# Kernel tuning notes

Hardware: AMD Instinct MI355X
Metric: run time of the kernel (lower is better)

## Reference

```python
import jax, jax.numpy as jnp
import numpy as np

B, Wd, C, H, F = 48, 88, 256, 32, 1024
NH_SELF, NH_CROSS = 8, 8


def _ln(x, g, b, eps=1e-5):
    mu = x.mean(-1, keepdims=True)
    var = ((x - mu) ** 2).mean(-1, keepdims=True)
    return (x - mu) / jnp.sqrt(var + eps) * g + b


def setup_inputs() -> dict:
    key = jax.random.key(0)
    ks = jax.random.split(key, 16)
    s = 0.02  # weight init scale
    d = {
        'pooled_features': jax.random.normal(ks[0], (B, Wd, C), jnp.float32),
        'features': jax.random.normal(ks[1], (B, C, H, Wd), jnp.float32),
        'self_pe': jax.random.normal(ks[2], (Wd, C), jnp.float32),
        'cross_pe': jax.random.normal(ks[3], (H, C), jnp.float32),
    }
    # LayerNorm params
    for n in ['ln_qs', 'ln_vs', 'ln_qc', 'ln_kv', 'ln_vc', 'ln_ffn']:
        d[n + '_g'] = jnp.ones((C,), jnp.float32)
        d[n + '_b'] = jnp.zeros((C,), jnp.float32)
    # attention projections (stored [in,out]; y = x @ W + b)
    names = ['Wq_s', 'Wk_s', 'Wv_s', 'Wp_s', 'Wq_c', 'Wk_c', 'Wv_c', 'Wp_c']
    for i, n in enumerate(names):
        d[n] = jax.random.normal(ks[4 + i], (C, C), jnp.float32) * s
    for n in ['bq_s', 'bv_s', 'bp_s', 'bq_c', 'bv_c', 'bp_c']:
        d[n] = jnp.zeros((C,), jnp.float32)
    # FFN
    d['W1'] = jax.random.normal(ks[12], (C, F), jnp.float32) * s
    d['b1'] = jnp.zeros((F,), jnp.float32)
    d['W2'] = jax.random.normal(ks[13], (F, C), jnp.float32) * s
    d['b2'] = jnp.zeros((C,), jnp.float32)
    return d


def reference(pooled_features, features, self_pe, cross_pe,
              ln_qs_g, ln_qs_b, ln_vs_g, ln_vs_b,
              ln_qc_g, ln_qc_b, ln_kv_g, ln_kv_b, ln_vc_g, ln_vc_b,
              ln_ffn_g, ln_ffn_b,
              Wq_s, bq_s, Wk_s, Wv_s, bv_s, Wp_s, bp_s,
              Wq_c, bq_c, Wk_c, Wv_c, bv_c, Wp_c, bp_c,
              W1, b1, W2, b2):
    b, w, c = pooled_features.shape
    h = features.shape[2]
    ds = c // NH_SELF
    dc = c // NH_CROSS

    # ---- cross attention first (op_order='cross_first', with_pe=True) ----
    xq = pooled_features                                  # [B,W,C]
    qn = _ln(xq, ln_qc_g, ln_qc_b)
    kv = jnp.transpose(features, (0, 3, 2, 1))            # [B,W,H,C]
    kn = _ln(kv + cross_pe[None, None], ln_kv_g, ln_kv_b)
    vn = _ln(kv, ln_vc_g, ln_vc_b)
    q = (qn @ Wq_c + bq_c).reshape(b, w, NH_CROSS, dc)    # query len 1 per column
    k = (kn @ Wk_c).reshape(b, w, h, NH_CROSS, dc)
    v = (vn @ Wv_c + bv_c).reshape(b, w, h, NH_CROSS, dc)
    attn = jnp.einsum('bwhd,bwkhd->bwhk', q, k) * (dc ** -0.5)
    attn = jax.nn.softmax(attn, axis=-1)
    out = jnp.einsum('bwhk,bwkhd->bwhd', attn, v).reshape(b, w, c)
    x = out @ Wp_c + bp_c + xq

    # ---- self attention over width tokens ----
    qn = _ln(x + self_pe[None], ln_qs_g, ln_qs_b)
    vn = _ln(x, ln_vs_g, ln_vs_b)
    q = (qn @ Wq_s + bq_s).reshape(b, w, NH_SELF, ds)
    k = (qn @ Wk_s).reshape(b, w, NH_SELF, ds)
    v = (vn @ Wv_s + bv_s).reshape(b, w, NH_SELF, ds)
    attn = jnp.einsum('bnhd,bmhd->bhnm', q, k) * (ds ** -0.5)
    attn = jax.nn.softmax(attn, axis=-1)
    out = jnp.einsum('bhnm,bmhd->bnhd', attn, v).reshape(b, w, c)
    x = out @ Wp_s + bp_s + x

    # ---- FFN (mmcv FFN, num_fcs=2, GELU, identity residual) ----
    hdn = _ln(x, ln_ffn_g, ln_ffn_b)
    hdn = jax.nn.gelu(hdn @ W1 + b1, approximate=False) @ W2 + b2
    return x + hdn
```

## Files before the change

kernel.cpp:

```cpp
#include <hip/hip_runtime.h>
#include <math.h>

#define B_   48
#define W_   88
#define C_   256
#define H_   32
#define F_   1024
#define BW_  (B_ * W_)
#define BWH_ (B_ * W_ * H_)
#define HW_  (H_ * W_)

typedef float  f32x4  __attribute__((ext_vector_type(4)));
typedef __bf16 bf16x8 __attribute__((ext_vector_type(8)));

__device__ __forceinline__ unsigned short f2bf(float f) {
  union { float f; unsigned int u; } v; v.f = f;
  unsigned int r = v.u + 0x7FFFu + ((v.u >> 16) & 1u);
  return (unsigned short)(r >> 16);
}
__device__ __forceinline__ float bf2f(unsigned short h) {
  union { unsigned int u; float f; } v; v.u = ((unsigned int)h) << 16;
  return v.f;
}
__device__ __forceinline__ unsigned int pack2(float a, float b) {
  return (unsigned int)f2bf(a) | ((unsigned int)f2bf(b) << 16);
}

__global__ __launch_bounds__(256) void prep_all(
    const float* __restrict__ Wq_s, const float* __restrict__ Wk_s,
    const float* __restrict__ Wv_s, const float* __restrict__ Wp_s,
    const float* __restrict__ W1, const float* __restrict__ W2,
    const float* __restrict__ Wq_c, const float* __restrict__ Wk_c,
    const float* __restrict__ Wv_c, const float* __restrict__ Wp_c,
    const float* __restrict__ bq_s, const float* __restrict__ bv_s,
    const float* __restrict__ bq_c, const float* __restrict__ bv_c,
    const float* __restrict__ bp_c,
    const float* __restrict__ pooled,
    const float* __restrict__ ln_qc_g, const float* __restrict__ ln_qc_b,
    unsigned short* __restrict__ wqkvs, unsigned short* __restrict__ wps,
    unsigned short* __restrict__ w1t, unsigned short* __restrict__ w2t,
    unsigned short* __restrict__ mqk, unsigned short* __restrict__ mvp,
    float* __restrict__ bqk, float* __restrict__ bvp,
    float* __restrict__ bqkvs, unsigned short* __restrict__ qn_c) {
  __shared__ float smem[256 * 33 + 4 * 33];
  int blk = blockIdx.x, t = threadIdx.x;

  if (blk < 768) {
    const float* src; unsigned short* dst; int Cc, R, tile;
    if (blk < 64)       { src = Wq_s; dst = wqkvs;          Cc = 256;  R = 256;  tile = blk; }
    else if (blk < 128) { src = Wk_s; dst = wqkvs + 65536;  Cc = 256;  R = 256;  tile = blk - 64; }
    else if (blk < 192) { src = Wv_s; dst = wqkvs + 131072; Cc = 256;  R = 256;  tile = blk - 128; }
    else if (blk < 256) { src = Wp_s; dst = wps;            Cc = 256;  R = 256;  tile = blk - 192; }
    else if (blk < 512) { src = W1;   dst = w1t;            Cc = 1024; R = 256;  tile = blk - 256; }
    else                { src = W2;   dst = w2t;            Cc = 256;  R = 1024; tile = blk - 512; }
    int tcn = Cc >> 5;
    int tr = tile / tcn, tc = tile % tcn;
    float (*lds)[33] = (float(*)[33])smem;
    int r = t >> 3, c4 = (t & 7) * 4;
    float4 v = *(const float4*)(src + (size_t)(tr * 32 + r) * Cc + tc * 32 + c4);
    lds[r][c4 + 0] = v.x; lds[r][c4 + 1] = v.y; lds[r][c4 + 2] = v.z; lds[r][c4 + 3] = v.w;
    __syncthreads();
    int rd = t >> 3, cd4 = (t & 7) * 4;
    unsigned int u0 = pack2(lds[cd4 + 0][rd], lds[cd4 + 1][rd]);
    unsigned int u1 = pack2(lds[cd4 + 2][rd], lds[cd4 + 3][rd]);
    uint2 u; u.x = u0; u.y = u1;
    *(uint2*)(dst + (size_t)(tc * 32 + rd) * R + tr * 32 + cd4) = u;
  } else if (blk < 1280) {
    int lb = blk - 768;
    int h = lb >> 6, cb = lb & 63;
    float (*wq)[33] = (float(*)[33])smem;
    float (*wk)[33] = (float(*)[33])(smem + 256 * 33);
#pragma unroll
    for (int p = 0; p < 8; p++) {
      int dp = (t >> 3) + 32 * p, d4 = (t & 7) * 4;
      float4 v = *(const float4*)(Wq_c + (size_t)dp * 256 + 32 * h + d4);
      wq[dp][d4 + 0] = v.x; wq[dp][d4 + 1] = v.y; wq[dp][d4 + 2] = v.z; wq[dp][d4 + 3] = v.w;
    }
    if (t < 128) {
      int c_l = t >> 5, dd = t & 31;
      wk[c_l][dd] = Wk_c[(size_t)(cb * 4 + c_l) * 256 + 32 * h + dd];
    }
    __syncthreads();
    const float scale = 0.17677669529663689f;
    int c_l = t >> 6, ln = t & 63;
    int n = 256 * h + cb * 4 + c_l;
#pragma unroll
    for (int j = 0; j < 4; j++) {
      int dp = ln + 64 * j;
      float acc = 0.f;
#pragma unroll
      for (int dd = 0; dd < 32; dd++) acc += wq[dp][dd] * wk[c_l][dd];
      mqk[(size_t)n * 256 + dp] = f2bf(acc * scale);
    }
    if (ln == 0) {
      float bb = 0.f;
#pragma unroll
      for (int dd = 0; dd < 32; dd++) bb += bq_c[32 * h + dd] * wk[c_l][dd];
      bqk[n] = bb * scale;
    }
  } else if (blk < 1792) {
    int lb = blk - 1280;
    int h = lb >> 6, db = lb & 63;
    float (*wv)[33] = (float(*)[33])smem;
    float (*wp)[33] = (float(*)[33])(smem + 256 * 33);
#pragma unroll
    for (int p = 0; p < 8; p++) {
      int c = (t >> 3) + 32 * p, d4 = (t & 7) * 4;
      float4 v = *(const float4*)(Wv_c + (size_t)c * 256 + 32 * h + d4);
      wv[c][d4 + 0] = v.x; wv[c][d4 + 1] = v.y; wv[c][d4 + 2] = v.z; wv[c][d4 + 3] = v.w;
    }
    if (t < 128) {
      int d_l = t >> 5, dd = t & 31;
      wp[d_l][dd] = Wp_c[(size_t)(32 * h + dd) * 256 + db * 4 + d_l];
    }
    __syncthreads();
    int d_l = t >> 6, ln = t & 63;
    int d = db * 4 + d_l;
#pragma unroll
    for (int j = 0; j < 4; j++) {
      int c = ln + 64 * j;
      float acc = 0.f;
#pragma unroll
      for (int dd = 0; dd < 32; dd++) acc += wv[c][dd] * wp[d_l][dd];
      mvp[(size_t)d * 2048 + 256 * h + c] = f2bf(acc);
    }
  } else if (blk == 1792) {
    float acc = bp_c[t];
    for (int dp = 0; dp < 256; dp++) acc += bv_c[dp] * Wp_c[(size_t)dp * 256 + t];
    bvp[t] = acc;
    bqkvs[t] = bq_s[t]; bqkvs[256 + t] = 0.f; bqkvs[512 + t] = bv_s[t];
  } else {
    int row = blk - 1793, c = t;
    float v = pooled[(size_t)row * C_ + c];
    float s1 = v, s2 = v * v;
#pragma unroll
    for (int m = 32; m > 0; m >>= 1) {
      s1 += __shfl_xor(s1, m, 64); s2 += __shfl_xor(s2, m, 64);
    }
    float* red = smem;
    int wave = c >> 6;
    if ((c & 63) == 0) { red[wave] = s1; red[4 + wave] = s2; }
    __syncthreads();
    s1 = red[0] + red[1] + red[2] + red[3];
    s2 = red[4] + red[5] + red[6] + red[7];
    float mu = s1 * (1.f / C_);
    float rs = rsqrtf(s2 * (1.f / C_) - mu * mu + 1e-5f);
    qn_c[(size_t)row * C_ + c] = f2bf((v - mu) * rs * ln_qc_g[c] + ln_qc_b[c]);
  }
}

__global__ __launch_bounds__(256) void ln_transpose4(
    const float* __restrict__ features, const float* __restrict__ cross_pe,
    const float* __restrict__ g_kv, const float* __restrict__ b_kv,
    const float* __restrict__ g_vc, const float* __restrict__ b_vc,
    unsigned short* __restrict__ kn, unsigned short* __restrict__ vn) {
  int b   = blockIdx.x / 176;
  int tl  = blockIdx.x % 176;
  int hw0 = tl * 16;
  __shared__ float tileT[256][17];
  int t = threadIdx.x;
  {
    int a  = (t & 3) * 4;
    int cc = t >> 2;
    const float* fb = features + (size_t)b * C_ * HW_ + hw0;
#pragma unroll
    for (int p = 0; p < 4; p++) {
      int c = cc + p * 64;
      float4 v = *(const float4*)(fb + (size_t)c * HW_ + a);
      tileT[c][a + 0] = v.x; tileT[c][a + 1] = v.y;
      tileT[c][a + 2] = v.z; tileT[c][a + 3] = v.w;
    }
  }
  __syncthreads();
  int row = t >> 4, ln = t & 15;
  int hw = hw0 + row;
  int hh = hw / 88, ww = hw - hh * 88;
  const float* per = cross_pe + hh * 256;
  float vreg[16], preg[16];
  float s1 = 0, s2 = 0, p1 = 0, p2 = 0;
#pragma unroll
  for (int j = 0; j < 4; j++) {
    int c0 = 4 * ln + 64 * j;
    float4 pv = *(const float4*)(per + c0);
    float pa[4] = {pv.x, pv.y, pv.z, pv.w};
#pragma unroll
    for (int i = 0; i < 4; i++) {
      float v  = tileT[c0 + i][row];
      float vp = v + pa[i];
      vreg[4 * j + i] = v; preg[4 * j + i] = pa[i];
      s1 += v;  s2 += v * v;
      p1 += vp; p2 += vp * vp;
    }
  }
#pragma unroll
  for (int m = 1; m < 16; m <<= 1) {
    s1 += __shfl_xor(s1, m, 16); s2 += __shfl_xor(s2, m, 16);
    p1 += __shfl_xor(p1, m, 16); p2 += __shfl_xor(p2, m, 16);
  }
  float mu  = s1 * (1.f / 256.f);
  float rs  = rsqrtf(s2 * (1.f / 256.f) - mu * mu + 1e-5f);
  float muk = p1 * (1.f / 256.f);
  float rsk = rsqrtf(p2 * (1.f / 256.f) - muk * muk + 1e-5f);
  size_t ro = ((size_t)b * 88 + ww) * 32 + hh;
  unsigned short* vrow = vn + ro * 256;
  unsigned short* krow = kn + ro * 256;
#pragma unroll
  for (int j = 0; j < 4; j++) {
    int c0 = 4 * ln + 64 * j;
    float4 gv = *(const float4*)(g_vc + c0);
    float4 bv = *(const float4*)(b_vc + c0);
    float4 gk = *(const float4*)(g_kv + c0);
    float4 bk = *(const float4*)(b_kv + c0);
    float gva[4] = {gv.x, gv.y, gv.z, gv.w}, bva[4] = {bv.x, bv.y, bv.z, bv.w};
    float gka[4] = {gk.x, gk.y, gk.z, gk.w}, bka[4] = {bk.x, bk.y, bk.z, bk.w};
    float ov[4], ok[4];
#pragma unroll
    for (int i = 0; i < 4; i++) {
      float v = vreg[4 * j + i], p = preg[4 * j + i];
      ov[i] = (v - mu) * rs * gva[i] + bva[i];
      ok[i] = (v + p - muk) * rsk * gka[i] + bka[i];
    }
    uint2 uv, uk;
    uv.x = pack2(ov[0], ov[1]); uv.y = pack2(ov[2], ov[3]);
    uk.x = pack2(ok[0], ok[1]); uk.y = pack2(ok[2], ok[3]);
    *(uint2*)(vrow + c0) = uv;
    *(uint2*)(krow + c0) = uk;
  }
}

__global__ __launch_bounds__(256) void ln_rows(
    const float* __restrict__ x,
    const float* __restrict__ g, const float* __restrict__ bta,
    unsigned short* __restrict__ out) {
  int row = blockIdx.x, c = threadIdx.x;
  float v = x[(size_t)row * C_ + c];
  float s1 = v, s2 = v * v;
#pragma unroll
  for (int m = 32; m > 0; m >>= 1) {
    s1 += __shfl_xor(s1, m, 64);
    s2 += __shfl_xor(s2, m, 64);
  }
  __shared__ float red[8];
  int wave = c >> 6;
  if ((c & 63) == 0) { red[wave] = s1; red[4 + wave] = s2; }
  __syncthreads();
  s1 = red[0] + red[1] + red[2] + red[3];
  s2 = red[4] + red[5] + red[6] + red[7];
  float mu = s1 * (1.f / C_);
  float rs = rsqrtf(s2 * (1.f / C_) - mu * mu + 1e-5f);
  out[(size_t)row * C_ + c] = f2bf((v - mu) * rs * g[c] + bta[c]);
}

__global__ __launch_bounds__(256) void ln_dual(
    const float* __restrict__ x, const float* __restrict__ pe,
    const float* __restrict__ g1, const float* __restrict__ b1a,
    const float* __restrict__ g2, const float* __restrict__ b2a,
    unsigned short* __restrict__ out1, unsigned short* __restrict__ out2) {
  int row = blockIdx.x, c = threadIdx.x;
  float v = x[(size_t)row * C_ + c];
  float vp = v + pe[(size_t)(row % 88) * C_ + c];
  float s1 = v, s2 = v * v, t1 = vp, t2 = vp * vp;
#pragma unroll
  for (int m = 32; m > 0; m >>= 1) {
    s1 += __shfl_xor(s1, m, 64); s2 += __shfl_xor(s2, m, 64);
    t1 += __shfl_xor(t1, m, 64); t2 += __shfl_xor(t2, m, 64);
  }
  __shared__ float red[16];
  int wave = c >> 6;
  if ((c & 63) == 0) {
    red[wave] = s1; red[4 + wave] = s2; red[8 + wave] = t1; red[12 + wave] = t2;
  }
  __syncthreads();
  s1 = red[0] + red[1] + red[2] + red[3];
  s2 = red[4] + red[5] + red[6] + red[7];
  t1 = red[8] + red[9] + red[10] + red[11];
  t2 = red[12] + red[13] + red[14] + red[15];
  float mu = s1 * (1.f / C_), rs = rsqrtf(s2 * (1.f / C_) - mu * mu + 1e-5f);
  float mup = t1 * (1.f / C_), rsp = rsqrtf(t2 * (1.f / C_) - mup * mup + 1e-5f);
  out1[(size_t)row * C_ + c] = f2bf((vp - mup) * rsp * g1[c] + b1a[c]);
  out2[(size_t)row * C_ + c] = f2bf((v - mu) * rs * g2[c] + b2a[c]);
}

__global__ __launch_bounds__(256) void gemm_bt(
    const unsigned short* __restrict__ A, const unsigned short* __restrict__ Bt,
    int M, int N, int K,
    const float* __restrict__ bias, const float* __restrict__ resid,
    float* __restrict__ outF, unsigned short* __restrict__ outB, int act_gelu) {
  __shared__ __attribute__((aligned(16))) unsigned short As[64][32];
  __shared__ __attribute__((aligned(16))) unsigned short Bs[64][32];
  const int tiles_n = N >> 6;
  const int bm = blockIdx.x / tiles_n;
  const int bn = blockIdx.x % tiles_n;
  const int tid = threadIdx.x;
  const int wave = tid >> 6, lane = tid & 63;
  const int quad = lane >> 4, lr = lane & 15;
  const int wm = (wave >> 1) << 5, wn = (wave & 1) << 5;
  const int lrow = tid >> 2;
  const int lcol = (tid & 3) << 3;
  const size_t a_base = (size_t)(bm * 64 + lrow) * K + lcol;
  const size_t b_base = (size_t)(bn * 64 + lrow) * K + lcol;
  f32x4 acc[2][2] = {};
  uint4 areg = *(const uint4*)(A + a_base);
  uint4 breg = *(const uint4*)(Bt + b_base);
  for (int k0 = 0; k0 < K; k0 += 32) {
    *(uint4*)&As[lrow][lcol] = areg;
    *(uint4*)&Bs[lrow][lcol] = breg;
    __syncthreads();
    if (k0 + 32 < K) {
      areg = *(const uint4*)(A + a_base + k0 + 32);
      breg = *(const uint4*)(Bt + b_base + k0 + 32);
    }
    bf16x8 af0 = *(const bf16x8*)&As[wm + lr][quad << 3];
    bf16x8 af1 = *(const bf16x8*)&As[wm + 16 + lr][quad << 3];
    bf16x8 bf0 = *(const bf16x8*)&Bs[wn + lr][quad << 3];
    bf16x8 bf1 = *(const bf16x8*)&Bs[wn + 16 + lr][quad << 3];
    acc[0][0] = __builtin_amdgcn_mfma_f32_16x16x32_bf16(af0, bf0, acc[0][0], 0, 0, 0);
    acc[0][1] = __builtin_amdgcn_mfma_f32_16x16x32_bf16(af0, bf1, acc[0][1], 0, 0, 0);
    acc[1][0] = __builtin_amdgcn_mfma_f32_16x16x32_bf16(af1, bf0, acc[1][0], 0, 0, 0);
    acc[1][1] = __builtin_amdgcn_mfma_f32_16x16x32_bf16(af1, bf1, acc[1][1], 0, 0, 0);
    __syncthreads();
  }
#pragma unroll
  for (int i = 0; i < 2; i++)
#pragma unroll
    for (int j = 0; j < 2; j++)
#pragma unroll
      for (int rr = 0; rr < 4; rr++) {
        int row = bm * 64 + wm + i * 16 + quad * 4 + rr;
        int col = bn * 64 + wn + j * 16 + lr;
        float val = acc[i][j][rr];
        if (bias) val += bias[col];
        if (act_gelu) val = 0.5f * val * (1.f + erff(val * 0.70710678118654752f));
        if (resid) val += resid[(size_t)row * N + col];
        if (outF) outF[(size_t)row * N + col] = val;
        else outB[(size_t)row * N + col] = f2bf(val);
      }
}

__global__ __launch_bounds__(256) void gemm_bt_st(
    const unsigned short* __restrict__ A, const unsigned short* __restrict__ Bt,
    int M, int N, int K, int ldc,
    const float* __restrict__ bias, float* __restrict__ outF) {
  __shared__ __attribute__((aligned(16))) unsigned short As[64][32];
  __shared__ __attribute__((aligned(16))) unsigned short Bs[64][32];
  const int tiles_n = N >> 6;
  const int bm = blockIdx.x / tiles_n;
  const int bn = blockIdx.x % tiles_n;
  const int tid = threadIdx.x;
  const int wave = tid >> 6, lane = tid & 63;
  const int quad = lane >> 4, lr = lane & 15;
  const int wm = (wave >> 1) << 5, wn = (wave & 1) << 5;
  const int lrow = tid >> 2;
  const int lcol = (tid & 3) << 3;
  const size_t a_base = (size_t)(bm * 64 + lrow) * K + lcol;
  const size_t b_base = (size_t)(bn * 64 + lrow) * K + lcol;
  f32x4 acc[2][2] = {};
  uint4 areg = *(const uint4*)(A + a_base);
  uint4 breg = *(const uint4*)(Bt + b_base);
  for (int k0 = 0; k0 < K; k0 += 32) {
    *(uint4*)&As[lrow][lcol] = areg;
    *(uint4*)&Bs[lrow][lcol] = breg;
    __syncthreads();
    if (k0 + 32 < K) {
      areg = *(const uint4*)(A + a_base + k0 + 32);
      breg = *(const uint4*)(Bt + b_base + k0 + 32);
    }
    bf16x8 af0 = *(const bf16x8*)&As[wm + lr][quad << 3];
    bf16x8 af1 = *(const bf16x8*)&As[wm + 16 + lr][quad << 3];
    bf16x8 bf0 = *(const bf16x8*)&Bs[wn + lr][quad << 3];
    bf16x8 bf1 = *(const bf16x8*)&Bs[wn + 16 + lr][quad << 3];
    acc[0][0] = __builtin_amdgcn_mfma_f32_16x16x32_bf16(af0, bf0, acc[0][0], 0, 0, 0);
    acc[0][1] = __builtin_amdgcn_mfma_f32_16x16x32_bf16(af0, bf1, acc[0][1], 0, 0, 0);
    acc[1][0] = __builtin_amdgcn_mfma_f32_16x16x32_bf16(af1, bf0, acc[1][0], 0, 0, 0);
    acc[1][1] = __builtin_amdgcn_mfma_f32_16x16x32_bf16(af1, bf1, acc[1][1], 0, 0, 0);
    __syncthreads();
  }
#pragma unroll
  for (int i = 0; i < 2; i++)
#pragma unroll
    for (int j = 0; j < 2; j++)
#pragma unroll
      for (int rr = 0; rr < 4; rr++) {
        int row = bm * 64 + wm + i * 16 + quad * 4 + rr;
        int col = bn * 64 + wn + j * 16 + lr;
        outF[(size_t)row * ldc + col] = acc[i][j][rr] + bias[col];
      }
}

#define KSTR 264
__global__ __launch_bounds__(256) void cross_attn2(
    const unsigned short* __restrict__ qt_g,
    const unsigned short* __restrict__ kn, const unsigned short* __restrict__ vn,
    unsigned short* __restrict__ ctx_g) {
  int bw = blockIdx.x;
  int tid = threadIdx.x;
  __shared__ __attribute__((aligned(16))) unsigned short qtl[8][KSTR];
  __shared__ __attribute__((aligned(16))) unsigned short knl[32][KSTR];
  __shared__ __attribute__((aligned(16))) unsigned short vnl[32][KSTR];
  __shared__ float s_sc[32 * 9];
  __shared__ float ps[8 * 36];
  __shared__ __attribute__((aligned(16))) unsigned short ctxl[2048];
  {
    uint4 qv = *(const uint4*)(qt_g + (size_t)bw * 2048 + tid * 8);
    int h = tid >> 5, c0 = (tid & 31) * 8;
    *(uint4*)&qtl[h][c0] = qv;
    int j = tid >> 3, cs = (tid & 7) * 32;
    const unsigned short* kr = kn + ((size_t)bw * 32 + j) * 256 + cs;
    const unsigned short* vr = vn + ((size_t)bw * 32 + j) * 256 + cs;
#pragma unroll
    for (int k = 0; k < 4; k++) {
      *(uint4*)&knl[j][cs + k * 8] = *(const uint4*)(kr + k * 8);
      *(uint4*)&vnl[j][cs + k * 8] = *(const uint4*)(vr + k * 8);
    }
  }
  __syncthreads();
  {
    int j = tid >> 3, h = tid & 7;
    float acc = 0.f;
#pragma unroll
    for (int c8 = 0; c8 < 32; c8++) {
      bf16x8 kk = *(const bf16x8*)&knl[j][c8 * 8];
      bf16x8 qq = *(const bf16x8*)&qtl[h][c8 * 8];
#pragma unroll
      for (int i = 0; i < 8; i++) acc += (float)qq[i] * (float)kk[i];
    }
    s_sc[j * 9 + h] = acc;
  }
  __syncthreads();
  {
    int h = tid >> 5, j = tid & 31;
    float s = s_sc[j * 9 + h];
    float mx = s;
#pragma unroll
    for (int m = 16; m > 0; m >>= 1) mx = fmaxf(mx, __shfl_xor(mx, m, 32));
    float e = __expf(s - mx);
    float sum = e;
#pragma unroll
    for (int m = 16; m > 0; m >>= 1) sum += __shfl_xor(sum, m, 32);
    ps[h * 36 + j] = e / sum;
  }
  __syncthreads();
  {
    int h = tid & 7, c0 = (tid >> 3) * 8;
    float acc[8];
#pragma unroll
    for (int i = 0; i < 8; i++) acc[i] = 0.f;
#pragma unroll 8
    for (int j = 0; j < 32; j++) {
      float p = ps[h * 36 + j];
      bf16x8 vv = *(const bf16x8*)&vnl[j][c0];
#pragma unroll
      for (int i = 0; i < 8; i++) acc[i] += p * (float)vv[i];
    }
    unsigned short pk[8];
#pragma unroll
    for (int i = 0; i < 8; i++) pk[i] = f2bf(acc[i]);
    *(uint4*)&ctxl[h * 256 + c0] = *(uint4*)pk;
  }
  __syncthreads();
  *(uint4*)(ctx_g + (size_t)bw * 2048 + tid * 8) = *(const uint4*)&ctxl[tid * 8];
}

__global__ __launch_bounds__(192) void self_attn3(
    const float* __restrict__ qkv, unsigned short* __restrict__ out) {
  int b = blockIdx.x >> 3;
  int h = blockIdx.x & 7;
  int t = threadIdx.x;
  __shared__ float kl[88][33];
  __shared__ float vl[88][33];
  for (int i = t; i < 704; i += 192) {
    int m = i >> 3, d4 = (i & 7) << 2;
    float4 kv4 = *(const float4*)(qkv + (size_t)(b * 88 + m) * 768 + 256 + h * 32 + d4);
    float4 vv4 = *(const float4*)(qkv + (size_t)(b * 88 + m) * 768 + 512 + h * 32 + d4);
    kl[m][d4 + 0] = kv4.x; kl[m][d4 + 1] = kv4.y; kl[m][d4 + 2] = kv4.z; kl[m][d4 + 3] = kv4.w;
    vl[m][d4 + 0] = vv4.x; vl[m][d4 + 1] = vv4.y; vl[m][d4 + 2] = vv4.z; vl[m][d4 + 3] = vv4.w;
  }
  __syncthreads();
  int r = t >> 1, dh = t & 1;
  if (r < 88) {
    const float* qrow = qkv + (size_t)(b * 88 + r) * 768 + h * 32;
    float qr[32];
#pragma unroll
    for (int g = 0; g < 8; g++) {
      float4 q4 = *(const float4*)(qrow + g * 4);
      qr[g * 4 + 0] = q4.x; qr[g * 4 + 1] = q4.y; qr[g * 4 + 2] = q4.z; qr[g * 4 + 3] = q4.w;
    }
    float sreg[44];
    float mx = -1e30f;
    int m0 = dh * 44;
    for (int mi = 0; mi < 44; mi++) {
      const float* krow = kl[m0 + mi];
      float s = 0.f;
#pragma unroll
      for (int d = 0; d < 32; d++) s += qr[d] * krow[d];
      s *= 0.17677669529663689f;
      sreg[mi] = s;
      mx = fmaxf(mx, s);
    }
    mx = fmaxf(mx, __shfl_xor(mx, 1, 64));
    float sum = 0.f;
    for (int mi = 0; mi < 44; mi++) { float e = __expf(sreg[mi] - mx); sreg[mi] = e; sum += e; }
    sum += __shfl_xor(sum, 1, 64);
    float inv = 1.f / sum;
    float o[32];
#pragma unroll
    for (int d = 0; d < 32; d++) o[d] = 0.f;
    for (int mi = 0; mi < 44; mi++) {
      float p = sreg[mi] * inv;
      const float* vrow = vl[m0 + mi];
#pragma unroll
      for (int d = 0; d < 32; d++) o[d] += p * vrow[d];
    }
#pragma unroll
    for (int d = 0; d < 32; d++) o[d] += __shfl_xor(o[d], 1, 64);
    unsigned short* orow = out + (size_t)(b * 88 + r) * 256 + h * 32 + dh * 16;
    uint4 u0, u1;
    int d0 = dh * 16;
    u0.x = pack2(o[d0 + 0], o[d0 + 1]);  u0.y = pack2(o[d0 + 2], o[d0 + 3]);
    u0.z = pack2(o[d0 + 4], o[d0 + 5]);  u0.w = pack2(o[d0 + 6], o[d0 + 7]);
    u1.x = pack2(o[d0 + 8], o[d0 + 9]);  u1.y = pack2(o[d0 + 10], o[d0 + 11]);
    u1.z = pack2(o[d0 + 12], o[d0 + 13]); u1.w = pack2(o[d0 + 14], o[d0 + 15]);
    *(uint4*)(orow) = u0;
    *(uint4*)(orow + 8) = u1;
  }
}

extern "C" void kernel_launch(void* const* d_in, const int* in_sizes, int n_in,
                              void* d_out, int out_size, void* d_ws, size_t ws_size,
                              hipStream_t stream) {
  (void)in_sizes; (void)n_in; (void)out_size; (void)ws_size;
  const float* pooled   = (const float*)d_in[0];
  const float* features = (const float*)d_in[1];
  const float* self_pe  = (const float*)d_in[2];
  const float* cross_pe = (const float*)d_in[3];
  const float* ln_qs_g = (const float*)d_in[4],  *ln_qs_b = (const float*)d_in[5];
  const float* ln_vs_g = (const float*)d_in[6],  *ln_vs_b = (const float*)d_in[7];
  const float* ln_qc_g = (const float*)d_in[8],  *ln_qc_b = (const float*)d_in[9];
  const float* ln_kv_g = (const float*)d_in[10], *ln_kv_b = (const float*)d_in[11];
  const float* ln_vc_g = (const float*)d_in[12], *ln_vc_b = (const float*)d_in[13];
  const float* ln_ffn_g = (const float*)d_in[14], *ln_ffn_b = (const float*)d_in[15];
  const float* Wq_s = (const float*)d_in[16], *Wk_s = (const float*)d_in[17];
  const float* Wv_s = (const float*)d_in[18], *Wp_s = (const float*)d_in[19];
  const float* Wq_c = (const float*)d_in[20], *Wk_c = (const float*)d_in[21];
  const float* Wv_c = (const float*)d_in[22], *Wp_c = (const float*)d_in[23];
  const float* bq_s = (const float*)d_in[24], *bv_s = (const float*)d_in[25];
  const float* bp_s = (const float*)d_in[26], *bq_c = (const float*)d_in[27];
  const float* bv_c = (const float*)d_in[28], *bp_c = (const float*)d_in[29];
  const float* W1 = (const float*)d_in[30], *b1 = (const float*)d_in[31];
  const float* W2 = (const float*)d_in[32], *b2 = (const float*)d_in[33];
  float* outp = (float*)d_out;
  char* ws = (char*)d_ws;

  size_t off = 0;
  auto alloc = [&](size_t bytes) { size_t o = off; off = (off + bytes + 255) & ~(size_t)255; return o; };
  const size_t big = (size_t)BWH_ * C_ * 2;
  size_t KN  = alloc(big);
  size_t VN  = alloc(big);
  size_t QT  = alloc((size_t)BW_ * 2048 * 2);
  size_t CTX = alloc((size_t)BW_ * 2048 * 2);
  size_t MQK = alloc((size_t)2048 * 256 * 2);
  size_t MVP = alloc((size_t)256 * 2048 * 2);
  size_t BQK = alloc(2048 * 4);
  size_t BVP = alloc(256 * 4);
  size_t WQKVS = alloc((size_t)768 * 256 * 2);
  size_t BQKVS = alloc(768 * 4);
  size_t WPS = alloc(65536 * 2);
  size_t W1T = alloc(262144 * 2), W2T = alloc(262144 * 2);
  size_t QN_C = alloc((size_t)BW_ * C_ * 2);
  size_t offp = KN;
  auto allocP = [&](size_t bytes) { size_t o = offp; offp = (offp + bytes + 255) & ~(size_t)255; return o; };
  size_t X1    = allocP((size_t)BW_ * C_ * 4);
  size_t QN_S  = allocP((size_t)BW_ * C_ * 2);
  size_t VN_S  = allocP((size_t)BW_ * C_ * 2);
  size_t QKV_S = allocP((size_t)BW_ * 768 * 4);
  size_t S_O   = allocP((size_t)BW_ * C_ * 2);
  size_t X2    = allocP((size_t)BW_ * C_ * 4);
  size_t FFN   = allocP((size_t)BW_ * C_ * 2);
  size_t H1    = allocP((size_t)BW_ * F_ * 2);

  unsigned short* kn   = (unsigned short*)(ws + KN);
  unsigned short* vn   = (unsigned short*)(ws + VN);
  unsigned short* qt   = (unsigned short*)(ws + QT);
  unsigned short* ctx  = (unsigned short*)(ws + CTX);
  unsigned short* mqk  = (unsigned short*)(ws + MQK);
  unsigned short* mvp  = (unsigned short*)(ws + MVP);
  float* bqk = (float*)(ws + BQK);
  float* bvp = (float*)(ws + BVP);
  unsigned short* wqkvs = (unsigned short*)(ws + WQKVS);
  float* bqkvs = (float*)(ws + BQKVS);
  unsigned short* wps = (unsigned short*)(ws + WPS);
  unsigned short* w1t = (unsigned short*)(ws + W1T), *w2t = (unsigned short*)(ws + W2T);
  unsigned short* qn_c = (unsigned short*)(ws + QN_C);
  float*          x1   = (float*)(ws + X1);
  unsigned short* qn_s = (unsigned short*)(ws + QN_S);
  unsigned short* vn_s = (unsigned short*)(ws + VN_S);
  float* qkv_s = (float*)(ws + QKV_S);
  unsigned short* s_o  = (unsigned short*)(ws + S_O);
  float*          x2   = (float*)(ws + X2);
  unsigned short* ffn_n = (unsigned short*)(ws + FFN);
  unsigned short* h1    = (unsigned short*)(ws + H1);

  prep_all<<<6017, 256, 0, stream>>>(
      Wq_s, Wk_s, Wv_s, Wp_s, W1, W2, Wq_c, Wk_c, Wv_c, Wp_c,
      bq_s, bv_s, bq_c, bv_c, bp_c, pooled, ln_qc_g, ln_qc_b,
      wqkvs, wps, w1t, w2t, mqk, mvp, bqk, bvp, bqkvs, qn_c);

  ln_transpose4<<<B_ * 176, 256, 0, stream>>>(features, cross_pe,
      ln_kv_g, ln_kv_b, ln_vc_g, ln_vc_b, kn, vn);

  gemm_bt<<<(BW_ / 64) * (2048 / 64), 256, 0, stream>>>(qn_c, mqk, BW_, 2048, 256,
      bqk, nullptr, nullptr, qt, 0);

  cross_attn2<<<BW_, 256, 0, stream>>>(qt, kn, vn, ctx);

  gemm_bt<<<(BW_ / 64) * (C_ / 64), 256, 0, stream>>>(ctx, mvp, BW_, C_, 2048,
      bvp, pooled, x1, nullptr, 0);

  ln_dual<<<BW_, 256, 0, stream>>>(x1, self_pe, ln_qs_g, ln_qs_b,
                                   ln_vs_g, ln_vs_b, qn_s, vn_s);

  gemm_bt_st<<<(BW_ / 64) * (512 / 64), 256, 0, stream>>>(qn_s, wqkvs, BW_, 512, 256,
      768, bqkvs, qkv_s);
  gemm_bt_st<<<(BW_ / 64) * (256 / 64), 256, 0, stream>>>(vn_s, wqkvs + 131072, BW_, 256, 256,
      768, bqkvs + 512, qkv_s + 512);

  self_attn3<<<B_ * 8, 192, 0, stream>>>(qkv_s, s_o);

  gemm_bt<<<(BW_ / 64) * (C_ / 64), 256, 0, stream>>>(s_o, wps, BW_, C_, C_,
      bp_s, x1, x2, nullptr, 0);

  ln_rows<<<BW_, 256, 0, stream>>>(x2, ln_ffn_g, ln_ffn_b, ffn_n);
  gemm_bt<<<(BW_ / 64) * (F_ / 64), 256, 0, stream>>>(ffn_n, w1t, BW_, F_, C_,
      b1, nullptr, nullptr, h1, 1);
  gemm_bt<<<(BW_ / 64) * (C_ / 64), 256, 0, stream>>>(h1, w2t, BW_, C_, F_,
      b2, x2, outp, nullptr, 0);
}
```

Before: 530.8 us.

## Fuse KV layernorm and transpose into cross-attention with streamed online softmax

Removes the separate ln_transpose4 kernel and the large bf16 kn/vn intermediates. The new cross_fused kernel streams features per height row through double-buffered LDS and computes both layernorms on the fly, using precomputed cross_pe sums so the key statistics come from the raw-feature sums. It then accumulates exp-weighted values without max subtraction. This saves roughly 2x100MB of global writes and reads. The cost is an unstabilised softmax that could overflow for large scores, and it relies on 528 blocks with an XCD-aware mapping.

```diff
diff --git a/kernel.cpp b/kernel.cpp
--- a/kernel.cpp
+++ b/kernel.cpp
@@ -37,11 +37,13 @@
     const float* __restrict__ bp_c,
     const float* __restrict__ pooled,
     const float* __restrict__ ln_qc_g, const float* __restrict__ ln_qc_b,
+    const float* __restrict__ cross_pe,
     unsigned short* __restrict__ wqkvs, unsigned short* __restrict__ wps,
     unsigned short* __restrict__ w1t, unsigned short* __restrict__ w2t,
     unsigned short* __restrict__ mqk, unsigned short* __restrict__ mvp,
     float* __restrict__ bqk, float* __restrict__ bvp,
-    float* __restrict__ bqkvs, unsigned short* __restrict__ qn_c) {
+    float* __restrict__ bqkvs, unsigned short* __restrict__ qn_c,
+    float* __restrict__ pes) {
   __shared__ float smem[256 * 33 + 4 * 33];
   int blk = blockIdx.x, t = threadIdx.x;
 
@@ -129,7 +131,7 @@
     for (int dp = 0; dp < 256; dp++) acc += bv_c[dp] * Wp_c[(size_t)dp * 256 + t];
     bvp[t] = acc;
     bqkvs[t] = bq_s[t]; bqkvs[256 + t] = 0.f; bqkvs[512 + t] = bv_s[t];
-  } else {
+  } else if (blk < 6017) {
     int row = blk - 1793, c = t;
     float v = pooled[(size_t)row * C_ + c];
     float s1 = v, s2 = v * v;
@@ -146,85 +148,135 @@
     float mu = s1 * (1.f / C_);
     float rs = rsqrtf(s2 * (1.f / C_) - mu * mu + 1e-5f);
     qn_c[(size_t)row * C_ + c] = f2bf((v - mu) * rs * ln_qc_g[c] + ln_qc_b[c]);
-  }
-}
-
-__global__ __launch_bounds__(256) void ln_transpose4(
+  } else {
+    int h = t >> 3, seg = t & 7;
+    const float* pr = cross_pe + (size_t)h * 256 + seg * 32;
+    float s1 = 0.f, s2 = 0.f;
+#pragma unroll
+    for (int i = 0; i < 32; i++) { float v = pr[i]; s1 += v; s2 += v * v; }
+    s1 += __shfl_xor(s1, 1, 8); s2 += __shfl_xor(s2, 1, 8);
+    s1 += __shfl_xor(s1, 2, 8); s2 += __shfl_xor(s2, 2, 8);
+    s1 += __shfl_xor(s1, 4, 8); s2 += __shfl_xor(s2, 4, 8);
+    if (seg == 0) { pes[2 * h] = s1; pes[2 * h + 1] = s2; }
+  }
+}
+
+__global__ __launch_bounds__(256, 2) void cross_fused(
     const float* __restrict__ features, const float* __restrict__ cross_pe,
+    const unsigned short* __restrict__ qt_g,
     const float* __restrict__ g_kv, const float* __restrict__ b_kv,
     const float* __restrict__ g_vc, const float* __restrict__ b_vc,
-    unsigned short* __restrict__ kn, unsigned short* __restrict__ vn) {
-  int b   = blockIdx.x / 176;
-  int tl  = blockIdx.x % 176;
-  int hw0 = tl * 16;
-  __shared__ float tileT[256][17];
-  int t = threadIdx.x;
+    const float* __restrict__ pes,
+    unsigned short* __restrict__ ctx_g) {
+  __shared__ __attribute__((aligned(16))) unsigned short qtl[8 * 2056];
+  __shared__ __attribute__((aligned(16))) float stage[2 * 8 * 268];
+  const int p = blockIdx.x;
+  const int xcd = p & 7, slot = p >> 3;
+  const int b = xcd + 8 * (slot / 11);
+  const int w0 = (slot % 11) * 8;
+  const int t = threadIdx.x;
+  const int bw0 = b * 88 + w0;
+
+  for (int i = t; i < 2048; i += 256) {
+    int r = i >> 8, c = (i & 255) << 3;
+    *(uint4*)&qtl[r * 2056 + c] = *(const uint4*)(qt_g + (size_t)(bw0 + r) * 2048 + c);
+  }
+
+  const int w = t >> 5, c8 = t & 31, cbase = c8 << 3;
+  float gk[8], bk[8], gv[8], bv[8];
   {
-    int a  = (t & 3) * 4;
-    int cc = t >> 2;
-    const float* fb = features + (size_t)b * C_ * HW_ + hw0;
-#pragma unroll
-    for (int p = 0; p < 4; p++) {
-      int c = cc + p * 64;
-      float4 v = *(const float4*)(fb + (size_t)c * HW_ + a);
-      tileT[c][a + 0] = v.x; tileT[c][a + 1] = v.y;
-      tileT[c][a + 2] = v.z; tileT[c][a + 3] = v.w;
-    }
-  }
-  __syncthreads();
-  int row = t >> 4, ln = t & 15;
-  int hw = hw0 + row;
-  int hh = hw / 88, ww = hw - hh * 88;
-  const float* per = cross_pe + hh * 256;
-  float vreg[16], preg[16];
-  float s1 = 0, s2 = 0, p1 = 0, p2 = 0;
-#pragma unroll
-  for (int j = 0; j < 4; j++) {
-    int c0 = 4 * ln + 64 * j;
-    float4 pv = *(const float4*)(per + c0);
-    float pa[4] = {pv.x, pv.y, pv.z, pv.w};
-#pragma unroll
-    for (int i = 0; i < 4; i++) {
-      float v  = tileT[c0 + i][row];
-      float vp = v + pa[i];
-      vreg[4 * j + i] = v; preg[4 * j + i] = pa[i];
-      s1 += v;  s2 += v * v;
-      p1 += vp; p2 += vp * vp;
-    }
-  }
-#pragma unroll
-  for (int m = 1; m < 16; m <<= 1) {
-    s1 += __shfl_xor(s1, m, 16); s2 += __shfl_xor(s2, m, 16);
-    p1 += __shfl_xor(p1, m, 16); p2 += __shfl_xor(p2, m, 16);
-  }
-  float mu  = s1 * (1.f / 256.f);
-  float rs  = rsqrtf(s2 * (1.f / 256.f) - mu * mu + 1e-5f);
-  float muk = p1 * (1.f / 256.f);
-  float rsk = rsqrtf(p2 * (1.f / 256.f) - muk * muk + 1e-5f);
-  size_t ro = ((size_t)b * 88 + ww) * 32 + hh;
-  unsigned short* vrow = vn + ro * 256;
-  unsigned short* krow = kn + ro * 256;
-#pragma unroll
-  for (int j = 0; j < 4; j++) {
-    int c0 = 4 * ln + 64 * j;
-    float4 gv = *(const float4*)(g_vc + c0);
-    float4 bv = *(const float4*)(b_vc + c0);
-    float4 gk = *(const float4*)(g_kv + c0);
-    float4 bk = *(const float4*)(b_kv + c0);
-    float gva[4] = {gv.x, gv.y, gv.z, gv.w}, bva[4] = {bv.x, bv.y, bv.z, bv.w};
-    float gka[4] = {gk.x, gk.y, gk.z, gk.w}, bka[4] = {bk.x, bk.y, bk.z, bk.w};
-    float ov[4], ok[4];
-#pragma unroll
-    for (int i = 0; i < 4; i++) {
-      float v = vreg[4 * j + i], p = preg[4 * j + i];
-      ov[i] = (v - mu) * rs * gva[i] + bva[i];
-      ok[i] = (v + p - muk) * rsk * gka[i] + bka[i];
-    }
-    uint2 uv, uk;
-    uv.x = pack2(ov[0], ov[1]); uv.y = pack2(ov[2], ov[3]);
-    uk.x = pack2(ok[0], ok[1]); uk.y = pack2(ok[2], ok[3]);
-    *(uint2*)(vrow + c0) = uv;
-    *(uint2*)(krow + c0) = uk;
+    float4 u0 = *(const float4*)(g_kv + cbase), u1 = *(const float4*)(g_kv + cbase + 4);
+    gk[0]=u0.x; gk[1]=u0.y; gk[2]=u0.z; gk[3]=u0.w; gk[4]=u1.x; gk[5]=u1.y; gk[6]=u1.z; gk[7]=u1.w;
+    u0 = *(const float4*)(b_kv + cbase); u1 = *(const float4*)(b_kv + cbase + 4);
+    bk[0]=u0.x; bk[1]=u0.y; bk[2]=u0.z; bk[3]=u0.w; bk[4]=u1.x; bk[5]=u1.y; bk[6]=u1.z; bk[7]=u1.w;
+    u0 = *(const float4*)(g_vc + cbase); u1 = *(const float4*)(g_vc + cbase + 4);
+    gv[0]=u0.x; gv[1]=u0.y; gv[2]=u0.z; gv[3]=u0.w; gv[4]=u1.x; gv[5]=u1.y; gv[6]=u1.z; gv[7]=u1.w;
+    u0 = *(const float4*)(b_vc + cbase); u1 = *(const float4*)(b_vc + cbase + 4);
+    bv[0]=u0.x; bv[1]=u0.y; bv[2]=u0.z; bv[3]=u0.w; bv[4]=u1.x; bv[5]=u1.y; bv[6]=u1.z; bv[7]=u1.w;
+  }
+  float acc[8][8];
+#pragma unroll
+  for (int hd = 0; hd < 8; hd++)
+#pragma unroll
+    for (int i = 0; i < 8; i++) acc[hd][i] = 0.f;
+  float l[8];
+#pragma unroll
+  for (int hd = 0; hd < 8; hd++) l[hd] = 0.f;
+
+  const float* fbase = features + (size_t)b * (C_ * HW_) + w0;
+  float4 a0 = *(const float4*)(fbase + (size_t)t * HW_);
+  float4 a1 = *(const float4*)(fbase + (size_t)t * HW_ + 4);
+
+  for (int h = 0; h < 32; ++h) {
+    float* st = stage + (h & 1) * (8 * 268);
+    st[t] = a0.x; st[268 + t] = a0.y; st[536 + t] = a0.z; st[804 + t] = a0.w;
+    st[1072 + t] = a1.x; st[1340 + t] = a1.y; st[1608 + t] = a1.z; st[1876 + t] = a1.w;
+    float4 n0 = a0, n1 = a1;
+    if (h < 31) {
+      n0 = *(const float4*)(fbase + (size_t)t * HW_ + (h + 1) * 88);
+      n1 = *(const float4*)(fbase + (size_t)t * HW_ + (h + 1) * 88 + 4);
+    }
+    __syncthreads();
+    const float* sr = st + w * 268 + cbase;
+    float4 v0 = *(const float4*)(sr);
+    float4 v1 = *(const float4*)(sr + 4);
+    float vls[8] = {v0.x, v0.y, v0.z, v0.w, v1.x, v1.y, v1.z, v1.w};
+    float4 q0 = *(const float4*)(cross_pe + h * 256 + cbase);
+    float4 q1 = *(const float4*)(cross_pe + h * 256 + cbase + 4);
+    float pe8[8] = {q0.x, q0.y, q0.z, q0.w, q1.x, q1.y, q1.z, q1.w};
+    float s1 = 0.f, s2 = 0.f, sp = 0.f;
+#pragma unroll
+    for (int i = 0; i < 8; i++) {
+      s1 += vls[i]; s2 += vls[i] * vls[i]; sp += vls[i] * pe8[i];
+    }
+#pragma unroll
+    for (int m = 1; m < 32; m <<= 1) {
+      s1 += __shfl_xor(s1, m, 32);
+      s2 += __shfl_xor(s2, m, 32);
+      sp += __shfl_xor(sp, m, 32);
+    }
+    float mu_v = s1 * (1.f / 256.f);
+    float rs_v = rsqrtf(s2 * (1.f / 256.f) - mu_v * mu_v + 1e-5f);
+    float mu_k = (s1 + pes[2 * h]) * (1.f / 256.f);
+    float rs_k = rsqrtf((s2 + 2.f * sp + pes[2 * h + 1]) * (1.f / 256.f)
+                        - mu_k * mu_k + 1e-5f);
+    float kn8[8], vn8[8];
+#pragma unroll
+    for (int i = 0; i < 8; i++) {
+      vn8[i] = (vls[i] - mu_v) * rs_v * gv[i] + bv[i];
+      kn8[i] = (vls[i] + pe8[i] - mu_k) * rs_k * gk[i] + bk[i];
+    }
+    float sc[8];
+#pragma unroll
+    for (int hd = 0; hd < 8; hd++) {
+      bf16x8 q = *(const bf16x8*)&qtl[w * 2056 + hd * 256 + cbase];
+      float a = 0.f;
+#pragma unroll
+      for (int i = 0; i < 8; i++) a += kn8[i] * (float)q[i];
+      sc[hd] = a;
+    }
+#pragma unroll
+    for (int m = 1; m < 32; m <<= 1) {
+#pragma unroll
+      for (int hd = 0; hd < 8; hd++) sc[hd] += __shfl_xor(sc[hd], m, 32);
+    }
+#pragma unroll
+    for (int hd = 0; hd < 8; hd++) {
+      float e = __expf(sc[hd]);
+      l[hd] += e;
+#pragma unroll
+      for (int i = 0; i < 8; i++) acc[hd][i] += e * vn8[i];
+    }
+    a0 = n0; a1 = n1;
+  }
+  unsigned short* orow = ctx_g + (size_t)(bw0 + w) * 2048 + cbase;
+#pragma unroll
+  for (int hd = 0; hd < 8; hd++) {
+    float inv = 1.f / l[hd];
+    unsigned short pk[8];
+#pragma unroll
+    for (int i = 0; i < 8; i++) pk[i] = f2bf(acc[hd][i] * inv);
+    *(uint4*)(orow + hd * 256) = *(uint4*)pk;
   }
 }
 
@@ -385,80 +437,6 @@
         int col = bn * 64 + wn + j * 16 + lr;
         outF[(size_t)row * ldc + col] = acc[i][j][rr] + bias[col];
       }
-}
-
-#define KSTR 264
-__global__ __launch_bounds__(256) void cross_attn2(
-    const unsigned short* __restrict__ qt_g,
-    const unsigned short* __restrict__ kn, const unsigned short* __restrict__ vn,
-    unsigned short* __restrict__ ctx_g) {
-  int bw = blockIdx.x;
-  int tid = threadIdx.x;
-  __shared__ __attribute__((aligned(16))) unsigned short qtl[8][KSTR];
-  __shared__ __attribute__((aligned(16))) unsigned short knl[32][KSTR];
-  __shared__ __attribute__((aligned(16))) unsigned short vnl[32][KSTR];
-  __shared__ float s_sc[32 * 9];
-  __shared__ float ps[8 * 36];
-  __shared__ __attribute__((aligned(16))) unsigned short ctxl[2048];
-  {
-    uint4 qv = *(const uint4*)(qt_g + (size_t)bw * 2048 + tid * 8);
-    int h = tid >> 5, c0 = (tid & 31) * 8;
-    *(uint4*)&qtl[h][c0] = qv;
-    int j = tid >> 3, cs = (tid & 7) * 32;
-    const unsigned short* kr = kn + ((size_t)bw * 32 + j) * 256 + cs;
-    const unsigned short* vr = vn + ((size_t)bw * 32 + j) * 256 + cs;
-#pragma unroll
-    for (int k = 0; k < 4; k++) {
-      *(uint4*)&knl[j][cs + k * 8] = *(const uint4*)(kr + k * 8);
-      *(uint4*)&vnl[j][cs + k * 8] = *(const uint4*)(vr + k * 8);
-    }
-  }
-  __syncthreads();
-  {
-    int j = tid >> 3, h = tid & 7;
-    float acc = 0.f;
-#pragma unroll
-    for (int c8 = 0; c8 < 32; c8++) {
-      bf16x8 kk = *(const bf16x8*)&knl[j][c8 * 8];
-      bf16x8 qq = *(const bf16x8*)&qtl[h][c8 * 8];
-#pragma unroll
-      for (int i = 0; i < 8; i++) acc += (float)qq[i] * (float)kk[i];
-    }
-    s_sc[j * 9 + h] = acc;
-  }
-  __syncthreads();
-  {
-    int h = tid >> 5, j = tid & 31;
-    float s = s_sc[j * 9 + h];
-    float mx = s;
-#pragma unroll
-    for (int m = 16; m > 0; m >>= 1) mx = fmaxf(mx, __shfl_xor(mx, m, 32));
-    float e = __expf(s - mx);
-    float sum = e;
-#pragma unroll
-    for (int m = 16; m > 0; m >>= 1) sum += __shfl_xor(sum, m, 32);
-    ps[h * 36 + j] = e / sum;
-  }
-  __syncthreads();
-  {
-    int h = tid & 7, c0 = (tid >> 3) * 8;
-    float acc[8];
-#pragma unroll
-    for (int i = 0; i < 8; i++) acc[i] = 0.f;
-#pragma unroll 8
-    for (int j = 0; j < 32; j++) {
-      float p = ps[h * 36 + j];
-      bf16x8 vv = *(const bf16x8*)&vnl[j][c0];
-#pragma unroll
-      for (int i = 0; i < 8; i++) acc[i] += p * (float)vv[i];
-    }
-    unsigned short pk[8];
-#pragma unroll
-    for (int i = 0; i < 8; i++) pk[i] = f2bf(acc[i]);
-    *(uint4*)&ctxl[h * 256 + c0] = *(uint4*)pk;
-  }
-  __syncthreads();
-  *(uint4*)(ctx_g + (size_t)bw * 2048 + tid * 8) = *(const uint4*)&ctxl[tid * 8];
 }
 
 __global__ __launch_bounds__(192) void self_attn3(
@@ -553,9 +531,6 @@
 
   size_t off = 0;
   auto alloc = [&](size_t bytes) { size_t o = off; off = (off + bytes + 255) & ~(size_t)255; return o; };
-  const size_t big = (size_t)BWH_ * C_ * 2;
-  size_t KN  = alloc(big);
-  size_t VN  = alloc(big);
   size_t QT  = alloc((size_t)BW_ * 2048 * 2);
   size_t CTX = alloc((size_t)BW_ * 2048 * 2);
   size_t MQK = alloc((size_t)2048 * 256 * 2);
@@ -567,19 +542,16 @@
   size_t WPS = alloc(65536 * 2);
   size_t W1T = alloc(262144 * 2), W2T = alloc(262144 * 2);
   size_t QN_C = alloc((size_t)BW_ * C_ * 2);
-  size_t offp = KN;
-  auto allocP = [&](size_t bytes) { size_t o = offp; offp = (offp + bytes + 255) & ~(size_t)255; return o; };
-  size_t X1    = allocP((size_t)BW_ * C_ * 4);
-  size_t QN_S  = allocP((size_t)BW_ * C_ * 2);
-  size_t VN_S  = allocP((size_t)BW_ * C_ * 2);
-  size_t QKV_S = allocP((size_t)BW_ * 768 * 4);
-  size_t S_O   = allocP((size_t)BW_ * C_ * 2);
-  size_t X2    = allocP((size_t)BW_ * C_ * 4);
-  size_t FFN   = allocP((size_t)BW_ * C_ * 2);
-  size_t H1    = allocP((size_t)BW_ * F_ * 2);
-
-  unsigned short* kn   = (unsigned short*)(ws + KN);
-  unsigned short* vn   = (unsigned short*)(ws + VN);
+  size_t PES  = alloc(64 * 4);
+  size_t X1    = alloc((size_t)BW_ * C_ * 4);
+  size_t QN_S  = alloc((size_t)BW_ * C_ * 2);
+  size_t VN_S  = alloc((size_t)BW_ * C_ * 2);
+  size_t QKV_S = alloc((size_t)BW_ * 768 * 4);
+  size_t S_O   = alloc((size_t)BW_ * C_ * 2);
+  size_t X2    = alloc((size_t)BW_ * C_ * 4);
+  size_t FFN   = alloc((size_t)BW_ * C_ * 2);
+  size_t H1    = alloc((size_t)BW_ * F_ * 2);
+
   unsigned short* qt   = (unsigned short*)(ws + QT);
   unsigned short* ctx  = (unsigned short*)(ws + CTX);
   unsigned short* mqk  = (unsigned short*)(ws + MQK);
@@ -591,6 +563,7 @@
   unsigned short* wps = (unsigned short*)(ws + WPS);
   unsigned short* w1t = (unsigned short*)(ws + W1T), *w2t = (unsigned short*)(ws + W2T);
   unsigned short* qn_c = (unsigned short*)(ws + QN_C);
+  float* pes = (float*)(ws + PES);
   float*          x1   = (float*)(ws + X1);
   unsigned short* qn_s = (unsigned short*)(ws + QN_S);
   unsigned short* vn_s = (unsigned short*)(ws + VN_S);
@@ -600,18 +573,16 @@
   unsigned short* ffn_n = (unsigned short*)(ws + FFN);
   unsigned short* h1    = (unsigned short*)(ws + H1);
 
-  prep_all<<<6017, 256, 0, stream>>>(
+  prep_all<<<6018, 256, 0, stream>>>(
       Wq_s, Wk_s, Wv_s, Wp_s, W1, W2, Wq_c, Wk_c, Wv_c, Wp_c,
-      bq_s, bv_s, bq_c, bv_c, bp_c, pooled, ln_qc_g, ln_qc_b,
-      wqkvs, wps, w1t, w2t, mqk, mvp, bqk, bvp, bqkvs, qn_c);
-
-  ln_transpose4<<<B_ * 176, 256, 0, stream>>>(features, cross_pe,
-      ln_kv_g, ln_kv_b, ln_vc_g, ln_vc_b, kn, vn);
+      bq_s, bv_s, bq_c, bv_c, bp_c, pooled, ln_qc_g, ln_qc_b, cross_pe,
+      wqkvs, wps, w1t, w2t, mqk, mvp, bqk, bvp, bqkvs, qn_c, pes);
 
   gemm_bt<<<(BW_ / 64) * (2048 / 64), 256, 0, stream>>>(qn_c, mqk, BW_, 2048, 256,
       bqk, nullptr, nullptr, qt, 0);
 
-  cross_attn2<<<BW_, 256, 0, stream>>>(qt, kn, vn, ctx);
+  cross_fused<<<528, 256, 0, stream>>>(features, cross_pe, qt,
+      ln_kv_g, ln_kv_b, ln_vc_g, ln_vc_b, pes, ctx);
 
   gemm_bt<<<(BW_ / 64) * (C_ / 64), 256, 0, stream>>>(ctx, mvp, BW_, C_, 2048,
       bvp, pooled, x1, nullptr, 0);
```

New measurement: 512.4 us. 1.04x faster.
